# Kernel tuning notes

Measured on AMD Instinct MI355X. Metric: run time of the kernel, lower is better.

Reference implementation:

```python
import jax, jax.numpy as jnp
import numpy as np

B, T, N_EMBD, H = 8, 2048, 1024, 128

def setup_inputs() -> dict:
    key = jax.random.key(0)
    k1, k2, k3, k4 = jax.random.split(key, 4)
    x = jax.random.normal(k1, (B, T, N_EMBD), dtype=jnp.float32)
    s = 1.0 / np.sqrt(N_EMBD).astype(np.float32)
    Wq = jax.random.normal(k2, (N_EMBD, H), dtype=jnp.float32) * s
    Wk = jax.random.normal(k3, (N_EMBD, H), dtype=jnp.float32) * s
    Wv = jax.random.normal(k4, (N_EMBD, H), dtype=jnp.float32) * s
    return {"x": x, "Wq": Wq, "Wk": Wk, "Wv": Wv}

def reference(x, Wq, Wk, Wv):
    # x: [B,T,C]; projections (no bias per init_kwargs)
    q = x @ Wq  # [B,T,H]
    k = x @ Wk  # [B,T,H]
    v = x @ Wv  # [B,T,H]
    scale = jnp.asarray(k.shape[-1], x.dtype) ** -0.5
    att = jnp.einsum('bth,bsh->bts', q, k) * scale  # [B,T,T]
    Tlen = x.shape[1]
    causal = jnp.tril(jnp.ones((Tlen, Tlen), dtype=bool))  # bias buffer tril mask
    att = jnp.where(causal, att, jnp.asarray(-jnp.inf, att.dtype))
    att = jax.nn.softmax(att, axis=-1)
    # dropout omitted (eval mode / deterministic reference)
    y = jnp.einsum('bts,bsh->bth', att, v)  # [B,T,H]
    return y
```

## Files before the change

kernel.cpp:

```cpp
#include <hip/hip_runtime.h>
#include <hip/hip_bf16.h>
#include <stdint.h>

#define BB 8
#define TT 2048
#define CC 1024
#define HH 128
#define VTP 2112

typedef __attribute__((ext_vector_type(8))) short bf16x8;
typedef __attribute__((ext_vector_type(8))) unsigned short u16x8;
typedef __attribute__((ext_vector_type(4))) float f32x4;
typedef __attribute__((ext_vector_type(8))) _Float16 h16x8;

static __device__ __forceinline__ unsigned short f2bf(float f) {
    union { float f; uint32_t u; } v; v.f = f;
    return (unsigned short)((v.u + 0x7fffu + ((v.u >> 16) & 1u)) >> 16);
}

#define GLOBAL_AS __attribute__((address_space(1)))
#define LDS_AS    __attribute__((address_space(3)))
static __device__ __forceinline__ void async16(const void* g, void* l) {
    __builtin_amdgcn_global_load_lds((const GLOBAL_AS void*)g, (LDS_AS void*)l, 16, 0, 0);
}

__global__ __launch_bounds__(256) void wconv(
    const float* __restrict__ Wq, const float* __restrict__ Wk,
    const float* __restrict__ Wv, unsigned short* __restrict__ Wb)
{
    int u = blockIdx.x * 256 + threadIdx.x;
    if (u >= 3 * 128 * 128) return;
    int kc = u & 127, n = (u >> 7) & 127, mat = u >> 14;
    const float* W = (mat == 0) ? Wq : (mat == 1) ? Wk : Wv;
    const float* s = W + (size_t)(kc * 8) * HH + n;
    u16x8 v;
    #pragma unroll
    for (int j = 0; j < 8; j++) v[j] = f2bf(s[(size_t)j * HH]);
    *(u16x8*)(Wb + ((size_t)mat * HH + n) * CC + kc * 8) = v;
}

#define BS_U16 4608
#define EQ_OFF 0
#define EK_OFF 8704
#define EV_OFF 17408
__global__ __launch_bounds__(512) void qkv_proj(
    const float* __restrict__ x, const unsigned short* __restrict__ Wb,
    unsigned short* __restrict__ Q, unsigned short* __restrict__ K,
    unsigned short* __restrict__ Vt)
{
    __shared__ __align__(16) unsigned short lds[29184];

    const int m0  = blockIdx.x * 64;
    const int tid = threadIdx.x;
    const int lane = tid & 63;
    const int w    = tid >> 6;
    const int qd   = lane >> 4;
    const int ln   = lane & 15;
    const int wm   = w & 1;
    const int wn   = w >> 1;

    f32x4 acc[2][6];
    #pragma unroll
    for (int i = 0; i < 2; i++)
        #pragma unroll
        for (int j = 0; j < 6; j++) acc[i][j] = (f32x4){0.f,0.f,0.f,0.f};

    const int xr = tid >> 3;
    const int xg = (tid & 7) * 8;

    float4 xf[2];
    {
        const float* s = x + (size_t)(m0 + xr) * CC + xg;
        xf[0] = ((const float4*)s)[0];
        xf[1] = ((const float4*)s)[1];
    }

    for (int k0 = 0; k0 < CC; k0 += 64) {
        {
            u16x8 v0;
            v0[0]=f2bf(xf[0].x); v0[1]=f2bf(xf[0].y); v0[2]=f2bf(xf[0].z); v0[3]=f2bf(xf[0].w);
            v0[4]=f2bf(xf[1].x); v0[5]=f2bf(xf[1].y); v0[6]=f2bf(xf[1].z); v0[7]=f2bf(xf[1].w);
            *(u16x8*)&lds[xr * 72 + xg] = v0;
        }
        #pragma unroll
        for (int i = 0; i < 6; i++) {
            int sb = i * 512 + w * 64;
            int slot = sb + lane;
            int row = slot >> 3, j = (slot & 7) ^ (row & 7);
            async16(Wb + (size_t)row * CC + k0 + j * 8, &lds[BS_U16 + sb * 8]);
        }
        __syncthreads();
        if (k0 + 64 < CC) {
            const float* s = x + (size_t)(m0 + xr) * CC + k0 + 64 + xg;
            xf[0] = ((const float4*)s)[0];
            xf[1] = ((const float4*)s)[1];
        }
        #pragma unroll
        for (int ks = 0; ks < 2; ks++) {
            bf16x8 a0 = *(const bf16x8*)&lds[(wm*32 + ln) * 72 + ks*32 + qd*8];
            bf16x8 a1 = *(const bf16x8*)&lds[(wm*32 + 16 + ln) * 72 + ks*32 + qd*8];
            #pragma unroll
            for (int nf = 0; nf < 6; nf++) {
                int row = wn * 96 + nf * 16 + ln;
                int ch  = (ks * 4 + qd) ^ (row & 7);
                bf16x8 b = *(const bf16x8*)&lds[BS_U16 + (row * 8 + ch) * 8];
                acc[0][nf] = __builtin_amdgcn_mfma_f32_16x16x32_bf16(a0, b, acc[0][nf], 0, 0, 0);
                acc[1][nf] = __builtin_amdgcn_mfma_f32_16x16x32_bf16(a1, b, acc[1][nf], 0, 0, 0);
            }
        }
        __syncthreads();
    }

    #pragma unroll
    for (int mf = 0; mf < 2; mf++)
        #pragma unroll
        for (int nf = 0; nf < 6; nf++) {
            int n = wn * 96 + nf * 16;
            int mat = n >> 7, hb = n & 127;
            #pragma unroll
            for (int r = 0; r < 4; r++) {
                unsigned short v = f2bf(acc[mf][nf][r]);
                int mrow = wm*32 + mf*16 + qd*4 + r;
                if (mat < 2) lds[(mat ? EK_OFF : EQ_OFF) + mrow * 136 + hb + ln] = v;
                else         lds[EV_OFF + (hb + ln) * 72 + mrow] = v;
            }
        }
    __syncthreads();
    {
        int rr = tid >> 3, c0 = (tid & 7) * 16;
        #pragma unroll
        for (int i = 0; i < 2; i++) {
            u16x8 vq = *(const u16x8*)&lds[EQ_OFF + rr * 136 + c0 + i * 8];
            *(u16x8*)(Q + (size_t)(m0 + rr) * HH + c0 + i * 8) = vq;
            u16x8 vk = *(const u16x8*)&lds[EK_OFF + rr * 136 + c0 + i * 8];
            *(u16x8*)(K + (size_t)(m0 + rr) * HH + c0 + i * 8) = vk;
        }
    }
    {
        int bb = m0 >> 11, t0 = m0 & (TT - 1);
        int hh = tid >> 2, tf = (tid & 3) * 16;
        #pragma unroll
        for (int i = 0; i < 2; i++) {
            u16x8 vv = *(const u16x8*)&lds[EV_OFF + hh * 72 + tf + i * 8];
            *(u16x8*)(Vt + ((size_t)bb * HH + hh) * VTP + t0 + tf + i * 8) = vv;
        }
    }
}

__global__ __launch_bounds__(512) void attn(
    const unsigned short* __restrict__ Q, const unsigned short* __restrict__ K,
    const unsigned short* __restrict__ Vt, float* __restrict__ out)
{
    extern __shared__ __align__(16) unsigned short dyn[];
    unsigned short* KsB = dyn;
    unsigned short* VsB = dyn + 32768;
    unsigned short* PsB = dyn + 65536;
    float*          Lp  = (float*)(dyn + 75776);

    const int tid  = threadIdx.x;
    const int lane = tid & 63;
    const int wave = tid >> 6;
    const int qd = lane >> 4;
    const int ln = lane & 15;
    const int qgrp = wave >> 2;
    const int kq   = wave & 3;

    const int bx = blockIdx.x;
    const int b  = bx & 7;
    const int qt = bx >> 3;
    const int qbase = qt * 64 + qgrp * 32;
    const int nst = (qt + 2) >> 1;

    const unsigned short* Qb = Q  + (size_t)b * TT * HH;
    const unsigned short* Kb = K  + (size_t)b * TT * HH;
    const unsigned short* Vb = Vt + (size_t)b * HH * VTP;

    bf16x8 aq[2][4];
    #pragma unroll
    for (int qs = 0; qs < 2; qs++)
        #pragma unroll
        for (int c = 0; c < 4; c++)
            aq[qs][c] = *(const bf16x8*)(Qb + (size_t)(qbase + qs*16 + ln) * HH + c * 32 + qd * 8);

    f32x4 O[2][8];
    float lsum[2][4];
    #pragma unroll
    for (int qs = 0; qs < 2; qs++) {
        #pragma unroll
        for (int h = 0; h < 8; h++) O[qs][h] = (f32x4){0.f,0.f,0.f,0.f};
        #pragma unroll
        for (int r = 0; r < 4; r++) lsum[qs][r] = 0.f;
    }

    const float sl   = 0.08838834764831843f * 1.4426950408889634f;
    const float M0L2 = 7.2134752044448f;
    unsigned short* ps = PsB + wave * 1280;

    #define STAGE(S0, BUF)                                                              \
        do {                                                                            \
            _Pragma("unroll")                                                           \
            for (int i = 0; i < 4; i++) {                                               \
                int sb = i * 512 + wave * 64;                                           \
                int slot = sb + lane;                                                   \
                int row = slot >> 4, jj = (slot & 15) ^ (row & 15);                     \
                async16(Kb + (size_t)((S0) + row) * HH + jj * 8,                        \
                        KsB + (size_t)(BUF) * 16384 + sb * 8);                          \
            }                                                                           \
            _Pragma("unroll")                                                           \
            for (int i = 0; i < 4; i++) {                                               \
                int sb = i * 512 + wave * 64;                                           \
                int slot = sb + lane;                                                   \
                int row = slot >> 4, jj = (slot & 15) ^ (row & 15);                     \
                async16(Vb + (size_t)row * VTP + (S0) + jj * 8,                         \
                        VsB + (size_t)(BUF) * 16384 + sb * 8);                          \
            }                                                                           \
        } while (0)

    STAGE(0, 0);
    for (int st = 0; st < nst; st++) {
        __syncthreads();
        if (st + 1 < nst) STAGE((st + 1) * 128, (st + 1) & 1);
        const int buf = st & 1;
        const unsigned short* Ks = KsB + (size_t)buf * 16384;
        const unsigned short* Vs = VsB + (size_t)buf * 16384;
        const int s0 = st * 128;

        f32x4 s[2][2];
        s[0][0] = (f32x4){0.f,0.f,0.f,0.f}; s[0][1] = (f32x4){0.f,0.f,0.f,0.f};
        s[1][0] = (f32x4){0.f,0.f,0.f,0.f}; s[1][1] = (f32x4){0.f,0.f,0.f,0.f};
        #pragma unroll
        for (int nt = 0; nt < 2; nt++) {
            int krow = kq * 32 + nt * 16;
            #pragma unroll
            for (int c = 0; c < 4; c++) {
                bf16x8 bk = *(const bf16x8*)&Ks[(krow + ln) * 128 + (((c*4 + qd) ^ ln)) * 8];
                s[0][nt] = __builtin_amdgcn_mfma_f32_16x16x32_bf16(aq[0][c], bk, s[0][nt], 0, 0, 0);
                s[1][nt] = __builtin_amdgcn_mfma_f32_16x16x32_bf16(aq[1][c], bk, s[1][nt], 0, 0, 0);
            }
        }
        #pragma unroll
        for (int qs = 0; qs < 2; qs++)
            #pragma unroll
            for (int nt = 0; nt < 2; nt++) {
                int col = s0 + kq * 32 + nt * 16 + ln;
                #pragma unroll
                for (int r = 0; r < 4; r++) {
                    int row = qbase + qs * 16 + qd * 4 + r;
                    float e = __builtin_amdgcn_exp2f(s[qs][nt][r] * sl - M0L2);
                    e = (col <= row) ? e : 0.f;
                    lsum[qs][r] += e;
                    ps[(qs*16 + qd*4 + r) * 40 + nt*16 + ln] = f2bf(e);
                }
            }
        bf16x8 ap0 = *(const bf16x8*)&ps[ln * 40 + qd * 8];
        bf16x8 ap1 = *(const bf16x8*)&ps[(16 + ln) * 40 + qd * 8];
        #pragma unroll
        for (int ht = 0; ht < 8; ht++) {
            int vrow = ht * 16 + ln;
            bf16x8 bv = *(const bf16x8*)&Vs[vrow * 128 + (((kq*4 + qd) ^ ln)) * 8];
            O[0][ht] = __builtin_amdgcn_mfma_f32_16x16x32_bf16(ap0, bv, O[0][ht], 0, 0, 0);
            O[1][ht] = __builtin_amdgcn_mfma_f32_16x16x32_bf16(ap1, bv, O[1][ht], 0, 0, 0);
        }
    }

    __syncthreads();
    #pragma unroll
    for (int qs = 0; qs < 2; qs++)
        #pragma unroll
        for (int r = 0; r < 4; r++) {
            float sum = lsum[qs][r];
            #pragma unroll
            for (int off = 1; off < 16; off <<= 1)
                sum += __shfl_xor(sum, off, 64);
            if (ln == 0) Lp[wave * 32 + qs*16 + qd*4 + r] = sum;
        }
    _Float16* om = (_Float16*)KsB + (size_t)wave * 32 * 128;
    #pragma unroll
    for (int qs = 0; qs < 2; qs++)
        #pragma unroll
        for (int ht = 0; ht < 8; ht++)
            #pragma unroll
            for (int r = 0; r < 4; r++)
                om[(qs*16 + qd*4 + r) * 128 + ht*16 + ln] = (_Float16)O[qs][ht][r];
    __syncthreads();

    {
        int row = tid >> 3, h0 = (tid & 7) * 16;
        int g = row >> 5, rl = row & 31;
        float L = Lp[(g*4 + 0)*32 + rl] + Lp[(g*4 + 1)*32 + rl]
                + Lp[(g*4 + 2)*32 + rl] + Lp[(g*4 + 3)*32 + rl];
        float inv = 1.0f / L;
        const _Float16* p0 = (const _Float16*)KsB + (size_t)(g*4 + 0) * 4096 + rl * 128 + h0;
        const _Float16* p1 = p0 + 4096;
        const _Float16* p2 = p1 + 4096;
        const _Float16* p3 = p2 + 4096;
        float* op = out + ((size_t)b * TT + qt * 64 + row) * HH + h0;
        #pragma unroll
        for (int i = 0; i < 4; i++) {
            float4 v;
            v.x = (((float)p0[i*4+0] + (float)p1[i*4+0]) + ((float)p2[i*4+0] + (float)p3[i*4+0])) * inv;
            v.y = (((float)p0[i*4+1] + (float)p1[i*4+1]) + ((float)p2[i*4+1] + (float)p3[i*4+1])) * inv;
            v.z = (((float)p0[i*4+2] + (float)p1[i*4+2]) + ((float)p2[i*4+2] + (float)p3[i*4+2])) * inv;
            v.w = (((float)p0[i*4+3] + (float)p1[i*4+3]) + ((float)p2[i*4+3] + (float)p3[i*4+3])) * inv;
            ((float4*)op)[i] = v;
        }
    }
    #undef STAGE
}

extern "C" void kernel_launch(void* const* d_in, const int* in_sizes, int n_in,
                              void* d_out, int out_size, void* d_ws, size_t ws_size,
                              hipStream_t stream) {
    const float* x  = (const float*)d_in[0];
    const float* Wq = (const float*)d_in[1];
    const float* Wk = (const float*)d_in[2];
    const float* Wv = (const float*)d_in[3];

    unsigned short* Wb = (unsigned short*)d_ws;
    unsigned short* Qw = Wb + (size_t)3 * HH * CC;
    unsigned short* Kw = Qw + (size_t)BB * TT * HH;
    unsigned short* Vw = Kw + (size_t)BB * TT * HH;

    static bool attr_done = false;
    if (!attr_done) {
        hipFuncSetAttribute((const void*)attn,
                            hipFuncAttributeMaxDynamicSharedMemorySize, 152576);
        attr_done = true;
    }

    wconv<<<dim3(192), 256, 0, stream>>>(Wq, Wk, Wv, Wb);
    qkv_proj<<<dim3(256), 512, 0, stream>>>(x, Wb, Qw, Kw, Vw);
    attn<<<dim3(256), 512, 152576, stream>>>(Qw, Kw, Vw, (float*)d_out);
}
```

Before: 149.6 us.

## Split attention KV range across two blocks per query tile and merge

```diff
diff --git a/kernel.cpp b/kernel.cpp
--- a/kernel.cpp
+++ b/kernel.cpp
@@ -149,7 +149,8 @@
 
 __global__ __launch_bounds__(512) void attn(
     const unsigned short* __restrict__ Q, const unsigned short* __restrict__ K,
-    const unsigned short* __restrict__ Vt, float* __restrict__ out)
+    const unsigned short* __restrict__ Vt, float* __restrict__ Op,
+    float* __restrict__ Lop)
 {
     extern __shared__ __align__(16) unsigned short dyn[];
     unsigned short* KsB = dyn;
@@ -165,11 +166,14 @@
     const int qgrp = wave >> 2;
     const int kq   = wave & 3;
 
-    const int bx = blockIdx.x;
-    const int b  = bx & 7;
-    const int qt = bx >> 3;
+    const int bx   = blockIdx.x;
+    const int part = bx >> 8;
+    const int u    = bx & 255;
+    const int b    = u & 7;
+    const int qt   = 31 - (u >> 3);
     const int qbase = qt * 64 + qgrp * 32;
     const int nst = (qt + 2) >> 1;
+    const int cnt = (nst - part + 1) >> 1;
 
     const unsigned short* Qb = Q  + (size_t)b * TT * HH;
     const unsigned short* Kb = K  + (size_t)b * TT * HH;
@@ -216,14 +220,14 @@
             }                                                                           \
         } while (0)
 
-    STAGE(0, 0);
-    for (int st = 0; st < nst; st++) {
+    if (cnt > 0) STAGE(part * 128, 0);
+    for (int it = 0; it < cnt; it++) {
         __syncthreads();
-        if (st + 1 < nst) STAGE((st + 1) * 128, (st + 1) & 1);
-        const int buf = st & 1;
+        if (it + 1 < cnt) STAGE((part + 2*(it + 1)) * 128, (it + 1) & 1);
+        const int buf = it & 1;
         const unsigned short* Ks = KsB + (size_t)buf * 16384;
         const unsigned short* Vs = VsB + (size_t)buf * 16384;
-        const int s0 = st * 128;
+        const int s0 = (part + 2*it) * 128;
 
         f32x4 s[2][2];
         s[0][0] = (f32x4){0.f,0.f,0.f,0.f}; s[0][1] = (f32x4){0.f,0.f,0.f,0.f};
@@ -274,14 +278,14 @@
                 sum += __shfl_xor(sum, off, 64);
             if (ln == 0) Lp[wave * 32 + qs*16 + qd*4 + r] = sum;
         }
-    _Float16* om = (_Float16*)KsB + (size_t)wave * 32 * 128;
+    float* om = (float*)dyn + (size_t)wave * 32 * 132;
     #pragma unroll
     for (int qs = 0; qs < 2; qs++)
         #pragma unroll
         for (int ht = 0; ht < 8; ht++)
             #pragma unroll
             for (int r = 0; r < 4; r++)
-                om[(qs*16 + qd*4 + r) * 128 + ht*16 + ln] = (_Float16)O[qs][ht][r];
+                om[(qs*16 + qd*4 + r) * 132 + ht*16 + ln] = O[qs][ht][r];
     __syncthreads();
 
     {
@@ -289,23 +293,48 @@
         int g = row >> 5, rl = row & 31;
         float L = Lp[(g*4 + 0)*32 + rl] + Lp[(g*4 + 1)*32 + rl]
                 + Lp[(g*4 + 2)*32 + rl] + Lp[(g*4 + 3)*32 + rl];
-        float inv = 1.0f / L;
-        const _Float16* p0 = (const _Float16*)KsB + (size_t)(g*4 + 0) * 4096 + rl * 128 + h0;
-        const _Float16* p1 = p0 + 4096;
-        const _Float16* p2 = p1 + 4096;
-        const _Float16* p3 = p2 + 4096;
-        float* op = out + ((size_t)b * TT + qt * 64 + row) * HH + h0;
+        const float* p0 = (const float*)dyn + (size_t)(g*4 + 0) * 32 * 132 + rl * 132 + h0;
+        const float* p1 = p0 + 32 * 132;
+        const float* p2 = p1 + 32 * 132;
+        const float* p3 = p2 + 32 * 132;
+        float* op = Op + ((size_t)bx * 64 + row) * 128 + h0;
         #pragma unroll
         for (int i = 0; i < 4; i++) {
             float4 v;
-            v.x = (((float)p0[i*4+0] + (float)p1[i*4+0]) + ((float)p2[i*4+0] + (float)p3[i*4+0])) * inv;
-            v.y = (((float)p0[i*4+1] + (float)p1[i*4+1]) + ((float)p2[i*4+1] + (float)p3[i*4+1])) * inv;
-            v.z = (((float)p0[i*4+2] + (float)p1[i*4+2]) + ((float)p2[i*4+2] + (float)p3[i*4+2])) * inv;
-            v.w = (((float)p0[i*4+3] + (float)p1[i*4+3]) + ((float)p2[i*4+3] + (float)p3[i*4+3])) * inv;
+            v.x = (p0[i*4+0] + p1[i*4+0]) + (p2[i*4+0] + p3[i*4+0]);
+            v.y = (p0[i*4+1] + p1[i*4+1]) + (p2[i*4+1] + p3[i*4+1]);
+            v.z = (p0[i*4+2] + p1[i*4+2]) + (p2[i*4+2] + p3[i*4+2]);
+            v.w = (p0[i*4+3] + p1[i*4+3]) + (p2[i*4+3] + p3[i*4+3]);
             ((float4*)op)[i] = v;
         }
+        if ((tid & 7) == 0) Lop[(size_t)bx * 64 + row] = L;
     }
     #undef STAGE
+}
+
+__global__ __launch_bounds__(512) void attn_merge(
+    const float* __restrict__ Op, const float* __restrict__ Lop,
+    float* __restrict__ out)
+{
+    const int m = blockIdx.x;
+    const int b = m & 7, qt = 31 - (m >> 3);
+    const int row = threadIdx.x >> 3, h0 = (threadIdx.x & 7) * 16;
+    const float* a = Op + ((size_t)m * 64 + row) * 128 + h0;
+    const float* c = Op + ((size_t)(m + 256) * 64 + row) * 128 + h0;
+    float L = Lop[(size_t)m * 64 + row] + Lop[(size_t)(m + 256) * 64 + row];
+    float inv = 1.0f / L;
+    float* op = out + ((size_t)b * TT + qt * 64 + row) * HH + h0;
+    #pragma unroll
+    for (int i = 0; i < 4; i++) {
+        float4 va = ((const float4*)a)[i];
+        float4 vc = ((const float4*)c)[i];
+        float4 v;
+        v.x = (va.x + vc.x) * inv;
+        v.y = (va.y + vc.y) * inv;
+        v.z = (va.z + vc.z) * inv;
+        v.w = (va.w + vc.w) * inv;
+        ((float4*)op)[i] = v;
+    }
 }
 
 extern "C" void kernel_launch(void* const* d_in, const int* in_sizes, int n_in,
@@ -320,6 +349,8 @@
     unsigned short* Qw = Wb + (size_t)3 * HH * CC;
     unsigned short* Kw = Qw + (size_t)BB * TT * HH;
     unsigned short* Vw = Kw + (size_t)BB * TT * HH;
+    float* Op  = (float*)(Vw + (size_t)BB * HH * VTP);
+    float* Lop = Op + (size_t)512 * 64 * 128;
 
     static bool attr_done = false;
     if (!attr_done) {
@@ -330,5 +361,6 @@
 
     wconv<<<dim3(192), 256, 0, stream>>>(Wq, Wk, Wv, Wb);
     qkv_proj<<<dim3(256), 512, 0, stream>>>(x, Wb, Qw, Kw, Vw);
-    attn<<<dim3(256), 512, 152576, stream>>>(Qw, Kw, Vw, (float*)d_out);
-}
+    attn<<<dim3(512), 512, 152576, stream>>>(Qw, Kw, Vw, Op, Lop);
+    attn_merge<<<dim3(256), 512, 0, stream>>>(Op, Lop, (float*)d_out);
+}
```

After: 150.0 us. No clear change (+0.3%).

## Store Q/K/V in MFMA-fragment layout and read directly from global in attention

Applied to the files above, without the earlier changes.

```diff
diff --git a/kernel.cpp b/kernel.cpp
--- a/kernel.cpp
+++ b/kernel.cpp
@@ -6,12 +6,10 @@
 #define TT 2048
 #define CC 1024
 #define HH 128
-#define VTP 2112
 
 typedef __attribute__((ext_vector_type(8))) short bf16x8;
 typedef __attribute__((ext_vector_type(8))) unsigned short u16x8;
 typedef __attribute__((ext_vector_type(4))) float f32x4;
-typedef __attribute__((ext_vector_type(8))) _Float16 h16x8;
 
 static __device__ __forceinline__ unsigned short f2bf(float f) {
     union { float f; uint32_t u; } v; v.f = f;
@@ -23,6 +21,7 @@
 static __device__ __forceinline__ void async16(const void* g, void* l) {
     __builtin_amdgcn_global_load_lds((const GLOBAL_AS void*)g, (LDS_AS void*)l, 16, 0, 0);
 }
+
 
 __global__ __launch_bounds__(256) void wconv(
     const float* __restrict__ Wq, const float* __restrict__ Wk,
@@ -45,8 +44,8 @@
 #define EV_OFF 17408
 __global__ __launch_bounds__(512) void qkv_proj(
     const float* __restrict__ x, const unsigned short* __restrict__ Wb,
-    unsigned short* __restrict__ Q, unsigned short* __restrict__ K,
-    unsigned short* __restrict__ Vt)
+    unsigned short* __restrict__ QF, unsigned short* __restrict__ KF,
+    unsigned short* __restrict__ VF)
 {
     __shared__ __align__(16) unsigned short lds[29184];
 
@@ -128,12 +127,16 @@
     __syncthreads();
     {
         int rr = tid >> 3, c0 = (tid & 7) * 16;
+        int kbg = (m0 + rr) >> 4, lnr = rr & 15;
         #pragma unroll
         for (int i = 0; i < 2; i++) {
+            int c8 = (c0 >> 3) + i;
+            int db = c8 >> 2, qdw = c8 & 3;
+            size_t a = ((size_t)kbg * 4 + db) * 512 + qdw * 128 + lnr * 8;
             u16x8 vq = *(const u16x8*)&lds[EQ_OFF + rr * 136 + c0 + i * 8];
-            *(u16x8*)(Q + (size_t)(m0 + rr) * HH + c0 + i * 8) = vq;
+            *(u16x8*)(QF + a) = vq;
             u16x8 vk = *(const u16x8*)&lds[EK_OFF + rr * 136 + c0 + i * 8];
-            *(u16x8*)(K + (size_t)(m0 + rr) * HH + c0 + i * 8) = vk;
+            *(u16x8*)(KF + a) = vk;
         }
     }
     {
@@ -141,46 +144,46 @@
         int hh = tid >> 2, tf = (tid & 3) * 16;
         #pragma unroll
         for (int i = 0; i < 2; i++) {
+            int k0 = t0 + tf + i * 8;
+            size_t a = (((size_t)(bb * 64 + (k0 >> 5))) * 8 + (hh >> 4)) * 512
+                     + ((k0 >> 3) & 3) * 128 + (hh & 15) * 8;
             u16x8 vv = *(const u16x8*)&lds[EV_OFF + hh * 72 + tf + i * 8];
-            *(u16x8*)(Vt + ((size_t)bb * HH + hh) * VTP + t0 + tf + i * 8) = vv;
-        }
-    }
-}
-
-__global__ __launch_bounds__(512) void attn(
-    const unsigned short* __restrict__ Q, const unsigned short* __restrict__ K,
-    const unsigned short* __restrict__ Vt, float* __restrict__ out)
+            *(u16x8*)(VF + a) = vv;
+        }
+    }
+}
+
+__global__ __launch_bounds__(256) void attn(
+    const unsigned short* __restrict__ QF, const unsigned short* __restrict__ KF,
+    const unsigned short* __restrict__ VF, float* __restrict__ out)
 {
-    extern __shared__ __align__(16) unsigned short dyn[];
-    unsigned short* KsB = dyn;
-    unsigned short* VsB = dyn + 32768;
-    unsigned short* PsB = dyn + 65536;
-    float*          Lp  = (float*)(dyn + 75776);
+    __shared__ __align__(16) _Float16 Om[4][32 * 128];
+    __shared__ __align__(16) unsigned short Ps[4][32 * 40];
+    __shared__ float Lp[4][32];
 
     const int tid  = threadIdx.x;
     const int lane = tid & 63;
     const int wave = tid >> 6;
     const int qd = lane >> 4;
     const int ln = lane & 15;
-    const int qgrp = wave >> 2;
-    const int kq   = wave & 3;
+    const int kq = wave;
 
     const int bx = blockIdx.x;
-    const int b  = bx & 7;
-    const int qt = bx >> 3;
-    const int qbase = qt * 64 + qgrp * 32;
-    const int nst = (qt + 2) >> 1;
-
-    const unsigned short* Qb = Q  + (size_t)b * TT * HH;
-    const unsigned short* Kb = K  + (size_t)b * TT * HH;
-    const unsigned short* Vb = Vt + (size_t)b * HH * VTP;
+    int b, qt;
+    if (bx < 256) { b = bx & 7;               qt = 63 - (bx >> 3); }
+    else          { int u = bx - 256; b = u & 7; qt = u >> 3; }
+    const int qbase = qt * 32;
+    const int nst = (qt + 4) >> 2;
 
     bf16x8 aq[2][4];
-    #pragma unroll
-    for (int qs = 0; qs < 2; qs++)
-        #pragma unroll
-        for (int c = 0; c < 4; c++)
-            aq[qs][c] = *(const bf16x8*)(Qb + (size_t)(qbase + qs*16 + ln) * HH + c * 32 + qd * 8);
+    {
+        const unsigned short* qp = QF + ((size_t)(b * 128 + qt * 2) * 4) * 512 + lane * 8;
+        #pragma unroll
+        for (int qs = 0; qs < 2; qs++)
+            #pragma unroll
+            for (int c = 0; c < 4; c++)
+                aq[qs][c] = *(const bf16x8*)(qp + (qs * 4 + c) * 512);
+    }
 
     f32x4 O[2][8];
     float lsum[2][4];
@@ -194,46 +197,24 @@
 
     const float sl   = 0.08838834764831843f * 1.4426950408889634f;
     const float M0L2 = 7.2134752044448f;
-    unsigned short* ps = PsB + wave * 1280;
-
-    #define STAGE(S0, BUF)                                                              \
-        do {                                                                            \
-            _Pragma("unroll")                                                           \
-            for (int i = 0; i < 4; i++) {                                               \
-                int sb = i * 512 + wave * 64;                                           \
-                int slot = sb + lane;                                                   \
-                int row = slot >> 4, jj = (slot & 15) ^ (row & 15);                     \
-                async16(Kb + (size_t)((S0) + row) * HH + jj * 8,                        \
-                        KsB + (size_t)(BUF) * 16384 + sb * 8);                          \
-            }                                                                           \
-            _Pragma("unroll")                                                           \
-            for (int i = 0; i < 4; i++) {                                               \
-                int sb = i * 512 + wave * 64;                                           \
-                int slot = sb + lane;                                                   \
-                int row = slot >> 4, jj = (slot & 15) ^ (row & 15);                     \
-                async16(Vb + (size_t)row * VTP + (S0) + jj * 8,                         \
-                        VsB + (size_t)(BUF) * 16384 + sb * 8);                          \
-            }                                                                           \
-        } while (0)
-
-    STAGE(0, 0);
+    unsigned short* ps = Ps[wave];
+
+    const unsigned short* kp = KF + (size_t)(b * 128 + kq * 2) * 2048 + lane * 8;
+    const unsigned short* vp = VF + (size_t)(b * 64 + kq) * 4096 + lane * 8;
+
     for (int st = 0; st < nst; st++) {
-        __syncthreads();
-        if (st + 1 < nst) STAGE((st + 1) * 128, (st + 1) & 1);
-        const int buf = st & 1;
-        const unsigned short* Ks = KsB + (size_t)buf * 16384;
-        const unsigned short* Vs = VsB + (size_t)buf * 16384;
         const int s0 = st * 128;
+        const unsigned short* kst = kp + (size_t)st * 16384;
+        const unsigned short* vst = vp + (size_t)st * 16384;
 
         f32x4 s[2][2];
         s[0][0] = (f32x4){0.f,0.f,0.f,0.f}; s[0][1] = (f32x4){0.f,0.f,0.f,0.f};
         s[1][0] = (f32x4){0.f,0.f,0.f,0.f}; s[1][1] = (f32x4){0.f,0.f,0.f,0.f};
         #pragma unroll
         for (int nt = 0; nt < 2; nt++) {
-            int krow = kq * 32 + nt * 16;
             #pragma unroll
             for (int c = 0; c < 4; c++) {
-                bf16x8 bk = *(const bf16x8*)&Ks[(krow + ln) * 128 + (((c*4 + qd) ^ ln)) * 8];
+                bf16x8 bk = *(const bf16x8*)(kst + nt * 2048 + c * 512);
                 s[0][nt] = __builtin_amdgcn_mfma_f32_16x16x32_bf16(aq[0][c], bk, s[0][nt], 0, 0, 0);
                 s[1][nt] = __builtin_amdgcn_mfma_f32_16x16x32_bf16(aq[1][c], bk, s[1][nt], 0, 0, 0);
             }
@@ -256,14 +237,12 @@
         bf16x8 ap1 = *(const bf16x8*)&ps[(16 + ln) * 40 + qd * 8];
         #pragma unroll
         for (int ht = 0; ht < 8; ht++) {
-            int vrow = ht * 16 + ln;
-            bf16x8 bv = *(const bf16x8*)&Vs[vrow * 128 + (((kq*4 + qd) ^ ln)) * 8];
+            bf16x8 bv = *(const bf16x8*)(vst + ht * 512);
             O[0][ht] = __builtin_amdgcn_mfma_f32_16x16x32_bf16(ap0, bv, O[0][ht], 0, 0, 0);
             O[1][ht] = __builtin_amdgcn_mfma_f32_16x16x32_bf16(ap1, bv, O[1][ht], 0, 0, 0);
         }
     }
 
-    __syncthreads();
     #pragma unroll
     for (int qs = 0; qs < 2; qs++)
         #pragma unroll
@@ -272,9 +251,9 @@
             #pragma unroll
             for (int off = 1; off < 16; off <<= 1)
                 sum += __shfl_xor(sum, off, 64);
-            if (ln == 0) Lp[wave * 32 + qs*16 + qd*4 + r] = sum;
-        }
-    _Float16* om = (_Float16*)KsB + (size_t)wave * 32 * 128;
+            if (ln == 0) Lp[wave][qs*16 + qd*4 + r] = sum;
+        }
+    _Float16* om = &Om[wave][0];
     #pragma unroll
     for (int qs = 0; qs < 2; qs++)
         #pragma unroll
@@ -286,15 +265,13 @@
 
     {
         int row = tid >> 3, h0 = (tid & 7) * 16;
-        int g = row >> 5, rl = row & 31;
-        float L = Lp[(g*4 + 0)*32 + rl] + Lp[(g*4 + 1)*32 + rl]
-                + Lp[(g*4 + 2)*32 + rl] + Lp[(g*4 + 3)*32 + rl];
+        float L = Lp[0][row] + Lp[1][row] + Lp[2][row] + Lp[3][row];
         float inv = 1.0f / L;
-        const _Float16* p0 = (const _Float16*)KsB + (size_t)(g*4 + 0) * 4096 + rl * 128 + h0;
-        const _Float16* p1 = p0 + 4096;
-        const _Float16* p2 = p1 + 4096;
-        const _Float16* p3 = p2 + 4096;
-        float* op = out + ((size_t)b * TT + qt * 64 + row) * HH + h0;
+        const _Float16* p0 = &Om[0][row * 128 + h0];
+        const _Float16* p1 = &Om[1][row * 128 + h0];
+        const _Float16* p2 = &Om[2][row * 128 + h0];
+        const _Float16* p3 = &Om[3][row * 128 + h0];
+        float* op = out + ((size_t)b * TT + qt * 32 + row) * HH + h0;
         #pragma unroll
         for (int i = 0; i < 4; i++) {
             float4 v;
@@ -305,7 +282,6 @@
             ((float4*)op)[i] = v;
         }
     }
-    #undef STAGE
 }
 
 extern "C" void kernel_launch(void* const* d_in, const int* in_sizes, int n_in,
@@ -317,18 +293,11 @@
     const float* Wv = (const float*)d_in[3];
 
     unsigned short* Wb = (unsigned short*)d_ws;
-    unsigned short* Qw = Wb + (size_t)3 * HH * CC;
-    unsigned short* Kw = Qw + (size_t)BB * TT * HH;
-    unsigned short* Vw = Kw + (size_t)BB * TT * HH;
-
-    static bool attr_done = false;
-    if (!attr_done) {
-        hipFuncSetAttribute((const void*)attn,
-                            hipFuncAttributeMaxDynamicSharedMemorySize, 152576);
-        attr_done = true;
-    }
+    unsigned short* QFw = Wb + (size_t)3 * HH * CC;
+    unsigned short* KFw = QFw + (size_t)BB * TT * HH;
+    unsigned short* VFw = KFw + (size_t)BB * TT * HH;
 
     wconv<<<dim3(192), 256, 0, stream>>>(Wq, Wk, Wv, Wb);
-    qkv_proj<<<dim3(256), 512, 0, stream>>>(x, Wb, Qw, Kw, Vw);
-    attn<<<dim3(256), 512, 152576, stream>>>(Qw, Kw, Vw, (float*)d_out);
-}
+    qkv_proj<<<dim3(256), 512, 0, stream>>>(x, Wb, QFw, KFw, VFw);
+    attn<<<dim3(512), 256, 0, stream>>>(QFw, KFw, VFw, (float*)d_out);
+}
```

Result: slower. 159.7 us (+6.7%).

## Switch attention to 32x32x16 MFMA with transposed S and register-resident P

Applied to the files above, without the earlier changes.

```diff
diff --git a/kernel.cpp b/kernel.cpp
--- a/kernel.cpp
+++ b/kernel.cpp
@@ -11,7 +11,7 @@
 typedef __attribute__((ext_vector_type(8))) short bf16x8;
 typedef __attribute__((ext_vector_type(8))) unsigned short u16x8;
 typedef __attribute__((ext_vector_type(4))) float f32x4;
-typedef __attribute__((ext_vector_type(8))) _Float16 h16x8;
+typedef __attribute__((ext_vector_type(16))) float f32x16;
 
 static __device__ __forceinline__ unsigned short f2bf(float f) {
     union { float f; uint32_t u; } v; v.f = f;
@@ -154,14 +154,13 @@
     extern __shared__ __align__(16) unsigned short dyn[];
     unsigned short* KsB = dyn;
     unsigned short* VsB = dyn + 32768;
-    unsigned short* PsB = dyn + 65536;
-    float*          Lp  = (float*)(dyn + 75776);
+    float*          Lp  = (float*)(dyn + 65536);
 
     const int tid  = threadIdx.x;
     const int lane = tid & 63;
     const int wave = tid >> 6;
-    const int qd = lane >> 4;
-    const int ln = lane & 15;
+    const int q32  = lane & 31;
+    const int hi   = lane >> 5;
     const int qgrp = wave >> 2;
     const int kq   = wave & 3;
 
@@ -175,26 +174,20 @@
     const unsigned short* Kb = K  + (size_t)b * TT * HH;
     const unsigned short* Vb = Vt + (size_t)b * HH * VTP;
 
-    bf16x8 aq[2][4];
-    #pragma unroll
-    for (int qs = 0; qs < 2; qs++)
-        #pragma unroll
-        for (int c = 0; c < 4; c++)
-            aq[qs][c] = *(const bf16x8*)(Qb + (size_t)(qbase + qs*16 + ln) * HH + c * 32 + qd * 8);
-
-    f32x4 O[2][8];
-    float lsum[2][4];
-    #pragma unroll
-    for (int qs = 0; qs < 2; qs++) {
-        #pragma unroll
-        for (int h = 0; h < 8; h++) O[qs][h] = (f32x4){0.f,0.f,0.f,0.f};
-        #pragma unroll
-        for (int r = 0; r < 4; r++) lsum[qs][r] = 0.f;
-    }
+    bf16x8 bq[8];
+    #pragma unroll
+    for (int hs = 0; hs < 8; hs++)
+        bq[hs] = *(const bf16x8*)(Qb + (size_t)(qbase + q32) * HH + hs * 16 + hi * 8);
+
+    f32x16 O[4];
+    #pragma unroll
+    for (int ht = 0; ht < 4; ht++)
+        #pragma unroll
+        for (int r = 0; r < 16; r++) O[ht][r] = 0.f;
+    float lsum = 0.f;
 
     const float sl   = 0.08838834764831843f * 1.4426950408889634f;
     const float M0L2 = 7.2134752044448f;
-    unsigned short* ps = PsB + wave * 1280;
 
     #define STAGE(S0, BUF)                                                              \
         do {                                                                            \
@@ -225,63 +218,59 @@
         const unsigned short* Vs = VsB + (size_t)buf * 16384;
         const int s0 = st * 128;
 
-        f32x4 s[2][2];
-        s[0][0] = (f32x4){0.f,0.f,0.f,0.f}; s[0][1] = (f32x4){0.f,0.f,0.f,0.f};
-        s[1][0] = (f32x4){0.f,0.f,0.f,0.f}; s[1][1] = (f32x4){0.f,0.f,0.f,0.f};
-        #pragma unroll
-        for (int nt = 0; nt < 2; nt++) {
-            int krow = kq * 32 + nt * 16;
-            #pragma unroll
-            for (int c = 0; c < 4; c++) {
-                bf16x8 bk = *(const bf16x8*)&Ks[(krow + ln) * 128 + (((c*4 + qd) ^ ln)) * 8];
-                s[0][nt] = __builtin_amdgcn_mfma_f32_16x16x32_bf16(aq[0][c], bk, s[0][nt], 0, 0, 0);
-                s[1][nt] = __builtin_amdgcn_mfma_f32_16x16x32_bf16(aq[1][c], bk, s[1][nt], 0, 0, 0);
-            }
-        }
-        #pragma unroll
-        for (int qs = 0; qs < 2; qs++)
-            #pragma unroll
-            for (int nt = 0; nt < 2; nt++) {
-                int col = s0 + kq * 32 + nt * 16 + ln;
-                #pragma unroll
-                for (int r = 0; r < 4; r++) {
-                    int row = qbase + qs * 16 + qd * 4 + r;
-                    float e = __builtin_amdgcn_exp2f(s[qs][nt][r] * sl - M0L2);
-                    e = (col <= row) ? e : 0.f;
-                    lsum[qs][r] += e;
-                    ps[(qs*16 + qd*4 + r) * 40 + nt*16 + ln] = f2bf(e);
-                }
-            }
-        bf16x8 ap0 = *(const bf16x8*)&ps[ln * 40 + qd * 8];
-        bf16x8 ap1 = *(const bf16x8*)&ps[(16 + ln) * 40 + qd * 8];
-        #pragma unroll
-        for (int ht = 0; ht < 8; ht++) {
-            int vrow = ht * 16 + ln;
-            bf16x8 bv = *(const bf16x8*)&Vs[vrow * 128 + (((kq*4 + qd) ^ ln)) * 8];
-            O[0][ht] = __builtin_amdgcn_mfma_f32_16x16x32_bf16(ap0, bv, O[0][ht], 0, 0, 0);
-            O[1][ht] = __builtin_amdgcn_mfma_f32_16x16x32_bf16(ap1, bv, O[1][ht], 0, 0, 0);
+        f32x16 s;
+        #pragma unroll
+        for (int r = 0; r < 16; r++) s[r] = 0.f;
+        const int krow = kq * 32 + q32;
+        #pragma unroll
+        for (int hs = 0; hs < 8; hs++) {
+            bf16x8 ak = *(const bf16x8*)&Ks[krow * 128 + (((hs*2 + hi) ^ (krow & 15))) * 8];
+            s = __builtin_amdgcn_mfma_f32_32x32x16_bf16(ak, bq[hs], s, 0, 0, 0);
+        }
+        float p[16];
+        #pragma unroll
+        for (int r = 0; r < 16; r++) {
+            int key = s0 + kq * 32 + (r & 3) + 8 * (r >> 2) + 4 * hi;
+            float e = __builtin_amdgcn_exp2f(s[r] * sl - M0L2);
+            e = (key <= qbase + q32) ? e : 0.f;
+            lsum += e;
+            p[r] = e;
+        }
+        unsigned int w0, w1, w2, w3, w4, w5, w6, w7;
+        asm("v_cvt_pk_bf16_f32 %0, %1, %2" : "=v"(w0) : "v"(p[0]),  "v"(p[1]));
+        asm("v_cvt_pk_bf16_f32 %0, %1, %2" : "=v"(w1) : "v"(p[2]),  "v"(p[3]));
+        asm("v_cvt_pk_bf16_f32 %0, %1, %2" : "=v"(w2) : "v"(p[4]),  "v"(p[5]));
+        asm("v_cvt_pk_bf16_f32 %0, %1, %2" : "=v"(w3) : "v"(p[6]),  "v"(p[7]));
+        asm("v_cvt_pk_bf16_f32 %0, %1, %2" : "=v"(w4) : "v"(p[8]),  "v"(p[9]));
+        asm("v_cvt_pk_bf16_f32 %0, %1, %2" : "=v"(w5) : "v"(p[10]), "v"(p[11]));
+        asm("v_cvt_pk_bf16_f32 %0, %1, %2" : "=v"(w6) : "v"(p[12]), "v"(p[13]));
+        asm("v_cvt_pk_bf16_f32 %0, %1, %2" : "=v"(w7) : "v"(p[14]), "v"(p[15]));
+        asm volatile("v_permlane32_swap_b32 %0, %1" : "+v"(w0), "+v"(w2));
+        asm volatile("v_permlane32_swap_b32 %0, %1" : "+v"(w1), "+v"(w3));
+        asm volatile("v_permlane32_swap_b32 %0, %1" : "+v"(w4), "+v"(w6));
+        asm volatile("v_permlane32_swap_b32 %0, %1" : "+v"(w5), "+v"(w7));
+        union { unsigned int u[4]; bf16x8 v; } pa0, pa1;
+        pa0.u[0] = w0; pa0.u[1] = w1; pa0.u[2] = w2; pa0.u[3] = w3;
+        pa1.u[0] = w4; pa1.u[1] = w5; pa1.u[2] = w6; pa1.u[3] = w7;
+        #pragma unroll
+        for (int ht = 0; ht < 4; ht++) {
+            const int vrow = ht * 32 + q32;
+            bf16x8 bv0 = *(const bf16x8*)&Vs[vrow * 128 + (((kq*4 + 0 + hi) ^ (vrow & 15))) * 8];
+            O[ht] = __builtin_amdgcn_mfma_f32_32x32x16_bf16(pa0.v, bv0, O[ht], 0, 0, 0);
+            bf16x8 bv1 = *(const bf16x8*)&Vs[vrow * 128 + (((kq*4 + 2 + hi) ^ (vrow & 15))) * 8];
+            O[ht] = __builtin_amdgcn_mfma_f32_32x32x16_bf16(pa1.v, bv1, O[ht], 0, 0, 0);
         }
     }
 
     __syncthreads();
-    #pragma unroll
-    for (int qs = 0; qs < 2; qs++)
-        #pragma unroll
-        for (int r = 0; r < 4; r++) {
-            float sum = lsum[qs][r];
-            #pragma unroll
-            for (int off = 1; off < 16; off <<= 1)
-                sum += __shfl_xor(sum, off, 64);
-            if (ln == 0) Lp[wave * 32 + qs*16 + qd*4 + r] = sum;
-        }
+    lsum += __shfl_xor(lsum, 32, 64);
+    if (hi == 0) Lp[wave * 32 + q32] = lsum;
     _Float16* om = (_Float16*)KsB + (size_t)wave * 32 * 128;
     #pragma unroll
-    for (int qs = 0; qs < 2; qs++)
-        #pragma unroll
-        for (int ht = 0; ht < 8; ht++)
-            #pragma unroll
-            for (int r = 0; r < 4; r++)
-                om[(qs*16 + qd*4 + r) * 128 + ht*16 + ln] = (_Float16)O[qs][ht][r];
+    for (int ht = 0; ht < 4; ht++)
+        #pragma unroll
+        for (int r = 0; r < 16; r++)
+            om[((r & 3) + 8 * (r >> 2) + 4 * hi) * 128 + ht * 32 + q32] = (_Float16)O[ht][r];
     __syncthreads();
 
     {
@@ -324,11 +313,11 @@
     static bool attr_done = false;
     if (!attr_done) {
         hipFuncSetAttribute((const void*)attn,
-                            hipFuncAttributeMaxDynamicSharedMemorySize, 152576);
+                            hipFuncAttributeMaxDynamicSharedMemorySize, 132096);
         attr_done = true;
     }
 
     wconv<<<dim3(192), 256, 0, stream>>>(Wq, Wk, Wv, Wb);
     qkv_proj<<<dim3(256), 512, 0, stream>>>(x, Wb, Qw, Kw, Vw);
-    attn<<<dim3(256), 512, 152576, stream>>>(Qw, Kw, Vw, (float*)d_out);
-}
+    attn<<<dim3(256), 512, 132096, stream>>>(Qw, Kw, Vw, (float*)d_out);
+}
```

New measurement: 145.5 us. 2.7% less time.
